# Kernel optimization log

Hardware: AMD Instinct MI355X
Metric: run time of the kernel (lower is better)

Reference implementation:

```python
import jax, jax.numpy as jnp
import numpy as np

FRAME_N = 8
PATCH = (180, 320)
NUM_ITERS = 2
CG_MAX_ITER = 200
CG_TOL = 1e-12
NOISE_LEVEL = 5e-10  # deterministic midpoint of sigma_range=[0, 1e-9]


@jax.custom_vjp
def ste(x):
    # straight-through binarizer: fwd = (x > 0).float(), bwd = hardtanh(grad)
    return (x > 0).astype(x.dtype)


def _ste_fwd(x):
    return ste(x), None


def _ste_bwd(_, g):
    return (jnp.clip(g, -1.0, 1.0),)


ste.defvjp(_ste_fwd, _ste_bwd)


def _afun(mask, x):
    # x: [F, H, W] -> y: [2, H, W]
    return jnp.stack([jnp.sum(mask * x, axis=0),
                      jnp.sum((1.0 / FRAME_N - mask) * x, axis=0)], axis=0)


def _atfun(mask, y):
    # y: [2, H, W] -> x: [F, H, W]
    return mask * y[0][None, :, :] + (1.0 / FRAME_N - mask) * y[1][None, :, :]


def _cg_solve(A, b_new):
    x0 = jnp.zeros_like(b_new)
    r0 = b_new - A(x0)
    p0 = r0
    d0 = jnp.sum(r0 * r0)
    done0 = jnp.array(False)

    def step(carry, _):
        x, r, p, d, done = carry
        Ap = A(p)
        alpha = d / jnp.sum(p * Ap)
        x_n = x + alpha * p
        r_n = r - alpha * Ap
        d_n = jnp.sum(r_n * r_n)
        beta = d_n / d
        p_n = beta * p + r_n  # matches torch p *= beta; p += z with z = r
        # freeze state once ||r|| < tol (emulates the torch `break`)
        x2 = jnp.where(done, x, x_n)
        r2 = jnp.where(done, r, r_n)
        p2 = jnp.where(done, p, p_n)
        d2 = jnp.where(done, d, d_n)
        done2 = done | (jnp.sqrt(d_n) < CG_TOL)
        return (x2, r2, p2, d2, done2), None

    step = jax.checkpoint(step)
    (x, _, _, _, _), _ = jax.lax.scan(step, (x0, r0, p0, d0, done0), None,
                                      length=CG_MAX_ITER)
    return x


def reference(frames, ce_weight, rho):
    mask = ste(ce_weight)                       # [F, H, W] binary code
    frames = frames[..., :PATCH[0], :PATCH[1]]  # crop (no-op at given shapes)
    b = _afun(mask, frames)                     # [2, H, W] coded blur pair
    noise = NOISE_LEVEL * jax.random.normal(jax.random.key(42), b.shape, b.dtype)
    b = b + noise
    rho_s = rho[0]

    A = lambda w: _atfun(mask, _afun(mask, w)) + rho_s * w

    x = jnp.repeat(b, FRAME_N // 2, axis=0)     # [F, H, W]
    z = x
    u = x
    for _ in range(NUM_ITERS):
        v = z - u
        b_new = _atfun(mask, b) + rho_s * v
        x = _cg_solve(A, b_new)
        # NOTE: original computes v_denoised = layer(x + u) but never uses it
        # and never updates z; the CNN output is dead code, so it is omitted.
        u = u + x - z
    return x


def setup_inputs() -> dict:
    key = jax.random.key(0)
    k1, k2, k3 = jax.random.split(key, 3)
    frames = jax.random.normal(k1, (FRAME_N, *PATCH), dtype=jnp.float32)
    # nn.init.uniform(ce_weight, a=-1, b=1)
    ce_weight = 2.0 * jax.random.uniform(k2, (FRAME_N, *PATCH), dtype=jnp.float32) - 1.0
    # nn.init.uniform(rho, a=0.0, b=0.1)
    rho = 0.1 * jax.random.uniform(k3, (1,), dtype=jnp.float32)
    return {"frames": frames, "ce_weight": ce_weight, "rho": rho}
```

## Files before the change

kernel.cpp:

```cpp
#include <hip/hip_runtime.h>

#define FRAME_N 8
#define NPIX (180 * 320)

__global__ void __launch_bounds__(256) admm_video_kernel(
    const float* __restrict__ frames,
    const float* __restrict__ ce,
    const float* __restrict__ rho_p,
    float* __restrict__ out)
{
    int pix = blockIdx.x * blockDim.x + threadIdx.x;
    if (pix >= NPIX) return;

    const double rho = (double)rho_p[0];

    double f[FRAME_N], m[FRAME_N], c[FRAME_N];
#pragma unroll
    for (int t = 0; t < FRAME_N; ++t) {
        f[t] = (double)frames[t * NPIX + pix];
        float w = ce[t * NPIX + pix];
        m[t] = (w > 0.0f) ? 1.0 : 0.0;
        c[t] = 0.125 - m[t];
    }

    double b0 = 0.0, b1 = 0.0;
#pragma unroll
    for (int t = 0; t < FRAME_N; ++t) {
        b0 += m[t] * f[t];
        b1 += c[t] * f[t];
    }

    double g00 = 0.0, g01 = 0.0, g11 = 0.0;
#pragma unroll
    for (int t = 0; t < FRAME_N; ++t) {
        g00 += m[t] * m[t];
        g01 += m[t] * c[t];
        g11 += c[t] * c[t];
    }
    const double s00 = rho + g00;
    const double s01 = g01;
    const double s11 = rho + g11;
    const double inv_det = 1.0 / (s00 * s11 - s01 * s01);
    const double inv_rho = 1.0 / rho;

    double atb[FRAME_N];
#pragma unroll
    for (int t = 0; t < FRAME_N; ++t) atb[t] = m[t] * b0 + c[t] * b1;

    double p0 = 0.0, p1 = 0.0;
#pragma unroll
    for (int t = 0; t < FRAME_N; ++t) { p0 += m[t] * atb[t]; p1 += c[t] * atb[t]; }
    double w0 = (s11 * p0 - s01 * p1) * inv_det;
    double w1 = (s00 * p1 - s01 * p0) * inv_det;
    double x1[FRAME_N];
#pragma unroll
    for (int t = 0; t < FRAME_N; ++t)
        x1[t] = (atb[t] - m[t] * w0 - c[t] * w1) * inv_rho;

    double v2[FRAME_N];
#pragma unroll
    for (int t = 0; t < FRAME_N; ++t) {
        double x0 = (t < 4) ? b0 : b1;
        v2[t] = atb[t] + rho * (x0 - x1[t]);
    }

    p0 = 0.0; p1 = 0.0;
#pragma unroll
    for (int t = 0; t < FRAME_N; ++t) { p0 += m[t] * v2[t]; p1 += c[t] * v2[t]; }
    w0 = (s11 * p0 - s01 * p1) * inv_det;
    w1 = (s00 * p1 - s01 * p0) * inv_det;
#pragma unroll
    for (int t = 0; t < FRAME_N; ++t)
        out[t * NPIX + pix] = (float)((v2[t] - m[t] * w0 - c[t] * w1) * inv_rho);
}

extern "C" void kernel_launch(void* const* d_in, const int* in_sizes, int n_in,
                              void* d_out, int out_size, void* d_ws, size_t ws_size,
                              hipStream_t stream) {
    const float* frames = (const float*)d_in[0];
    const float* ce     = (const float*)d_in[1];
    const float* rho    = (const float*)d_in[2];
    float* out = (float*)d_out;

    const int threads = 256;
    const int blocks = (NPIX + threads - 1) / threads;
    admm_video_kernel<<<blocks, threads, 0, stream>>>(frames, ce, rho, out);
}
```

Before: 9.902 us.

## Derive closed-form float32 per-pixel solve and vectorize loads with float4

Replaces the double-precision per-pixel 2x2 normal-equation evaluation with an algebraically simplified float32 closed form built from the mask count and first-half count. Each thread now handles four pixels through float4 loads and stores, and the block size drops to 64. This aims to cut FP64 arithmetic and memory instruction count. The trade-off is reduced precision, including possible cancellation in float32, plus fewer total threads.

```diff
diff --git a/kernel.cpp b/kernel.cpp
--- a/kernel.cpp
+++ b/kernel.cpp
@@ -2,87 +2,91 @@
 
 #define FRAME_N 8
 #define NPIX (180 * 320)
+#define NQ (NPIX / 4)
 
-__global__ void __launch_bounds__(256) admm_video_kernel(
-    const float* __restrict__ frames,
-    const float* __restrict__ ce,
+__global__ void __launch_bounds__(64) admm_video_kernel(
+    const float4* __restrict__ frames,
+    const float4* __restrict__ ce,
     const float* __restrict__ rho_p,
-    float* __restrict__ out)
+    float4* __restrict__ out)
 {
-    int pix = blockIdx.x * blockDim.x + threadIdx.x;
-    if (pix >= NPIX) return;
+    int q = blockIdx.x * blockDim.x + threadIdx.x;
+    if (q >= NQ) return;
 
-    const double rho = (double)rho_p[0];
+    const float rho = rho_p[0];
 
-    double f[FRAME_N], m[FRAME_N], c[FRAME_N];
+    float4 f4[FRAME_N], w4[FRAME_N], o4[FRAME_N];
 #pragma unroll
     for (int t = 0; t < FRAME_N; ++t) {
-        f[t] = (double)frames[t * NPIX + pix];
-        float w = ce[t * NPIX + pix];
-        m[t] = (w > 0.0f) ? 1.0 : 0.0;
-        c[t] = 0.125 - m[t];
+        f4[t] = frames[t * NQ + q];
+        w4[t] = ce[t * NQ + q];
     }
 
-    double b0 = 0.0, b1 = 0.0;
+    const float* fp = reinterpret_cast<const float*>(f4);
+    const float* wp = reinterpret_cast<const float*>(w4);
+    float* op = reinterpret_cast<float*>(o4);
+
 #pragma unroll
-    for (int t = 0; t < FRAME_N; ++t) {
-        b0 += m[t] * f[t];
-        b1 += c[t] * f[t];
+    for (int p = 0; p < 4; ++p) {
+        float sumf = 0.0f, b0 = 0.0f;
+        int k = 0, k0 = 0;
+        bool m[FRAME_N];
+#pragma unroll
+        for (int t = 0; t < FRAME_N; ++t) {
+            float fv = fp[t * 4 + p];
+            bool mv = wp[t * 4 + p] > 0.0f;
+            m[t] = mv;
+            sumf += fv;
+            b0 += mv ? fv : 0.0f;
+            k += mv ? 1 : 0;
+            k0 += (mv && t < 4) ? 1 : 0;
+        }
+        const float b1 = 0.125f * sumf - b0;
+        const float fk = (float)k;
+
+        const float s00 = rho + fk;
+        const float s01 = -0.875f * fk;
+        const float s11 = rho + 0.75f * fk + 0.125f;
+        const float det = rho * rho + rho * (1.75f * fk + 0.125f)
+                        + 0.015625f * fk * (8.0f - fk);
+        const float invdet = 1.0f / det;
+
+        const float a0 = (s11 * b0 - s01 * b1) * invdet;
+        const float a1 = (s00 * b1 - s01 * b0) * invdet;
+
+        const float k0f = (float)k0;
+        const float k1f = fk - k0f;
+        const float t0 = k0f * b0 + k1f * b1;
+        const float t1 = 0.5f * (b0 + b1) - t0;
+
+        const float r0 = b0 - rho * a0 - t0;
+        const float r1 = b1 - rho * a1 - t1;
+        const float be0 = (s11 * r0 - s01 * r1) * invdet;
+        const float be1 = (s00 * r1 - s01 * r0) * invdet;
+
+        const float base = 0.125f * be1;
+        const float dmb = be0 - be1;
+#pragma unroll
+        for (int t = 0; t < FRAME_N; ++t) {
+            float x0 = (t < 4) ? b0 : b1;
+            op[t * 4 + p] = x0 + base + (m[t] ? dmb : 0.0f);
+        }
     }
 
-    double g00 = 0.0, g01 = 0.0, g11 = 0.0;
-#pragma unroll
-    for (int t = 0; t < FRAME_N; ++t) {
-        g00 += m[t] * m[t];
-        g01 += m[t] * c[t];
-        g11 += c[t] * c[t];
-    }
-    const double s00 = rho + g00;
-    const double s01 = g01;
-    const double s11 = rho + g11;
-    const double inv_det = 1.0 / (s00 * s11 - s01 * s01);
-    const double inv_rho = 1.0 / rho;
-
-    double atb[FRAME_N];
-#pragma unroll
-    for (int t = 0; t < FRAME_N; ++t) atb[t] = m[t] * b0 + c[t] * b1;
-
-    double p0 = 0.0, p1 = 0.0;
-#pragma unroll
-    for (int t = 0; t < FRAME_N; ++t) { p0 += m[t] * atb[t]; p1 += c[t] * atb[t]; }
-    double w0 = (s11 * p0 - s01 * p1) * inv_det;
-    double w1 = (s00 * p1 - s01 * p0) * inv_det;
-    double x1[FRAME_N];
 #pragma unroll
     for (int t = 0; t < FRAME_N; ++t)
-        x1[t] = (atb[t] - m[t] * w0 - c[t] * w1) * inv_rho;
-
-    double v2[FRAME_N];
-#pragma unroll
-    for (int t = 0; t < FRAME_N; ++t) {
-        double x0 = (t < 4) ? b0 : b1;
-        v2[t] = atb[t] + rho * (x0 - x1[t]);
-    }
-
-    p0 = 0.0; p1 = 0.0;
-#pragma unroll
-    for (int t = 0; t < FRAME_N; ++t) { p0 += m[t] * v2[t]; p1 += c[t] * v2[t]; }
-    w0 = (s11 * p0 - s01 * p1) * inv_det;
-    w1 = (s00 * p1 - s01 * p0) * inv_det;
-#pragma unroll
-    for (int t = 0; t < FRAME_N; ++t)
-        out[t * NPIX + pix] = (float)((v2[t] - m[t] * w0 - c[t] * w1) * inv_rho);
+        out[t * NQ + q] = o4[t];
 }
 
 extern "C" void kernel_launch(void* const* d_in, const int* in_sizes, int n_in,
                               void* d_out, int out_size, void* d_ws, size_t ws_size,
                               hipStream_t stream) {
-    const float* frames = (const float*)d_in[0];
-    const float* ce     = (const float*)d_in[1];
-    const float* rho    = (const float*)d_in[2];
-    float* out = (float*)d_out;
+    const float4* frames = (const float4*)d_in[0];
+    const float4* ce     = (const float4*)d_in[1];
+    const float* rho     = (const float*)d_in[2];
+    float4* out = (float4*)d_out;
 
-    const int threads = 256;
-    const int blocks = (NPIX + threads - 1) / threads;
+    const int threads = 64;
+    const int blocks = (NQ + threads - 1) / threads;
     admm_video_kernel<<<blocks, threads, 0, stream>>>(frames, ce, rho, out);
 }
```

Result: no change. 9.872 us (-0.3%).
